# Performance work log

Measured on AMD Instinct MI355X. Metric: run time of the kernel, lower is better.

Reference implementation:

```python
import jax, jax.numpy as jnp
import numpy as np

NUM_HEADS = 16
LN_EPS = 1e-5


def pos_encoding(length, d):
    pos = jnp.arange(length, dtype=jnp.float32)[:, None]
    i = jnp.arange(d, dtype=jnp.float32)[None, :]
    angle = pos / jnp.power(10000.0, (2.0 * jnp.floor(i / 2.0)) / d)
    return jnp.where((jnp.arange(d) % 2) == 0, jnp.sin(angle), jnp.cos(angle))


def rel_shift(x):
    # x: (B, H, l, m) -> TXL shift trick
    b, h, l, m = x.shape
    x = jnp.concatenate([x, jnp.zeros((b, h, l, 1), x.dtype)], axis=-1)
    x = x.reshape(b, h, l * (m + 1))
    return x[:, :, l - 1:-1].reshape(b, h, l, m)


def layer_norm(x, g, b):
    mu = jnp.mean(x, axis=-1, keepdims=True)
    var = jnp.mean(jnp.square(x - mu), axis=-1, keepdims=True)
    return (x - mu) * jax.lax.rsqrt(var + LN_EPS) * g + b


def setup_inputs() -> dict:
    key = jax.random.key(0)
    B, S, M, D, L, V = 2, 1024, 1024, 1024, 4, 32000
    ks = jax.random.split(key, 32)
    s = 0.02
    d = {
        'inputs': jax.random.randint(ks[0], (B, S), 0, V, dtype=jnp.int32),
        'mems': jax.random.normal(ks[1], (L, B, M, D), jnp.float32),
        'emb': jax.random.normal(ks[2], (V, D), jnp.float32) * s,
        'Wq': jax.random.normal(ks[3], (L, D, D), jnp.float32) * s,
        'bq': jnp.zeros((L, D), jnp.float32),
        'Wke': jax.random.normal(ks[4], (L, D, D), jnp.float32) * s,
        'bke': jnp.zeros((L, D), jnp.float32),
        'Wkr': jax.random.normal(ks[5], (L, D, D), jnp.float32) * s,
        'bkr': jnp.zeros((L, D), jnp.float32),
        'Wv': jax.random.normal(ks[6], (L, D, D), jnp.float32) * s,
        'bv': jnp.zeros((L, D), jnp.float32),
        'Wo': jax.random.normal(ks[7], (L, D, D), jnp.float32) * s,
        'bo': jnp.zeros((L, D), jnp.float32),
        'ln1_g': jnp.ones((L, D), jnp.float32),
        'ln1_b': jnp.zeros((L, D), jnp.float32),
        'W1': jax.random.normal(ks[8], (L, D, D), jnp.float32) * s,
        'b1': jnp.zeros((L, D), jnp.float32),
        'W2': jax.random.normal(ks[9], (L, D, D), jnp.float32) * s,
        'b2': jnp.zeros((L, D), jnp.float32),
        'ln2_g': jnp.ones((L, D), jnp.float32),
        'ln2_b': jnp.zeros((L, D), jnp.float32),
        'Wh': jax.random.normal(ks[10], (D, D), jnp.float32) * s,
        'bh': jnp.zeros((D,), jnp.float32),
        'Wf': jax.random.normal(ks[11], (D, V), jnp.float32) * s,
        'bf': jnp.zeros((V,), jnp.float32),
        'next_mem_len': 1024,
    }
    return d


def reference(inputs, mems, emb, Wq, bq, Wke, bke, Wkr, bkr, Wv, bv, Wo, bo,
              ln1_g, ln1_b, W1, b1, W2, b2, ln2_g, ln2_b, Wh, bh, Wf, bf,
              next_mem_len):
    B, S = inputs.shape
    L, _, M, D = mems.shape
    T = M + S
    H = NUM_HEADS
    dh = D // H
    sqrt_dk = jnp.sqrt(jnp.float32(dh))

    rel_enc = pos_encoding(T, D)[::-1]  # (T, D), reversed
    # look-ahead mask: query i may attend key j iff j <= i + M
    mask = (jnp.arange(T)[None, :] > (jnp.arange(S)[:, None] + M)).astype(jnp.float32)
    mask = mask[None, None] * -1e9  # (1,1,S,T)

    x = emb[inputs] * jnp.sqrt(jnp.float32(D))  # (B,S,D)

    for l in range(L):
        x_tilde = jnp.concatenate([mems[l], x], axis=1)  # (B,T,D)
        q = (x @ Wq[l] + bq[l]).reshape(B, S, H, dh).transpose(0, 2, 1, 3)
        k = (x_tilde @ Wke[l] + bke[l]).reshape(B, T, H, dh).transpose(0, 2, 1, 3)
        v = (x_tilde @ Wv[l] + bv[l]).reshape(B, T, H, dh).transpose(0, 2, 1, 3)
        A = jnp.einsum('bhsd,bhtd->bhst', q, k)
        Qr = (rel_enc @ Wkr[l] + bkr[l]).reshape(T, H, dh).transpose(1, 0, 2)  # (H,T,dh)
        B_hat = jnp.einsum('bhsd,htd->bhst', q, Qr)
        score = (A + rel_shift(B_hat)) / sqrt_dk + mask
        attn = jax.nn.softmax(score, axis=-1)
        ctx = jnp.einsum('bhst,bhtd->bhsd', attn, v)
        ctx = ctx.transpose(0, 2, 1, 3).reshape(B, S, D)
        attn_out = ctx @ Wo[l] + bo[l]
        h1 = layer_norm(x + attn_out, ln1_g[l], ln1_b[l])
        ff = jax.nn.gelu(h1 @ W1[l] + b1[l], approximate=False) @ W2[l] + b2[l]
        x = layer_norm(h1 + ff, ln2_g[l], ln2_b[l])

    x = jax.nn.gelu(x @ Wh + bh, approximate=False)
    logits = x @ Wf + bf
    return logits
```

## Files before the change

### kernel.cpp

```cpp
#include <hip/hip_runtime.h>
#include <hip/hip_bf16.h>
#include <math.h>

typedef __attribute__((ext_vector_type(4))) float f32x4;
typedef __attribute__((ext_vector_type(8))) short s16x8;
typedef __attribute__((ext_vector_type(4))) short s16x4;

#define BB 2
#define SS 1024
#define MEM 1024
#define DD 1024
#define LL 4
#define VV 32000
#define TT 2048
#define NH 16
#define DH 64

__device__ __forceinline__ short f2bf(float f) {
    unsigned u = __float_as_uint(f);
    u += 0x7fffu + ((u >> 16) & 1u);
    return (short)(u >> 16);
}

__device__ __forceinline__ float gelu_f(float x) {
    return 0.5f * x * (1.0f + erff(x * 0.70710678118654752f));
}

__device__ __forceinline__ void gll16(const short* g, short* l) {
    __builtin_amdgcn_global_load_lds(
        (__attribute__((address_space(1))) void*)(short*)g,
        (__attribute__((address_space(3))) void*)l, 16, 0, 0);
}

template<int WM, int WN>
__global__ __launch_bounds__(256) void gemm_bf16(
    const short* __restrict__ A, const short* __restrict__ Bt,
    const float* __restrict__ bias, void* __restrict__ Cv,
    int N, int K, int act, int obf)
{
    constexpr int BM = WM * 32, BN = WN * 32;
    constexpr int NA = BM / 32, NB = BN / 32;
    __shared__ short a_s[BM * 64];
    __shared__ short b_s[BN * 64];
    const int tid  = threadIdx.x;
    const int lane = tid & 63;
    const int wave = tid >> 6;
    const int wr = wave >> 1, wc = wave & 1;
    const int fr = lane & 15, fg = lane >> 4;
    const size_t m0 = (size_t)blockIdx.y * BM;
    const size_t n0 = (size_t)blockIdx.x * BN;

    const short* gA[NA]; short* lA[NA];
    const short* gB[NB]; short* lB[NB];
    #pragma unroll
    for (int i = 0; i < NA; ++i) {
        const int s   = i * 256 + tid;
        const int row = (s >> 7) * 16 + (s & 15);
        const int kof = ((s >> 4) & 7) * 8;
        gA[i] = A + (m0 + row) * (size_t)K + kof;
        lA[i] = &a_s[s * 8];
    }
    #pragma unroll
    for (int i = 0; i < NB; ++i) {
        const int s   = i * 256 + tid;
        const int nn  = (s >> 7) * 16 + (s & 15);
        const int kof = ((s >> 4) & 7) * 8;
        gB[i] = Bt + (n0 + nn) * (size_t)K + kof;
        lB[i] = &b_s[s * 8];
    }

    f32x4 acc[WM][WN] = {};

    #pragma unroll
    for (int i = 0; i < NA; ++i) gll16(gA[i], lA[i]);
    #pragma unroll
    for (int i = 0; i < NB; ++i) gll16(gB[i], lB[i]);

    for (int k0 = 0; k0 < K; k0 += 64) {
        __syncthreads();
        s16x8 af[WM][2], bf[WN][2];
        #pragma unroll
        for (int mi = 0; mi < WM; ++mi)
            #pragma unroll
            for (int h = 0; h < 2; ++h)
                af[mi][h] = *(const s16x8*)&a_s[((wr*WM + mi)*128 + (h*4 + fg)*16 + fr) * 8];
        #pragma unroll
        for (int ni = 0; ni < WN; ++ni)
            #pragma unroll
            for (int h = 0; h < 2; ++h)
                bf[ni][h] = *(const s16x8*)&b_s[((wc*WN + ni)*128 + (h*4 + fg)*16 + fr) * 8];
        if (k0 + 64 < K) {
            __syncthreads();
            #pragma unroll
            for (int i = 0; i < NA; ++i) gll16(gA[i] + k0 + 64, lA[i]);
            #pragma unroll
            for (int i = 0; i < NB; ++i) gll16(gB[i] + k0 + 64, lB[i]);
        }
        #pragma unroll
        for (int mi = 0; mi < WM; ++mi)
            #pragma unroll
            for (int ni = 0; ni < WN; ++ni) {
                acc[mi][ni] = __builtin_amdgcn_mfma_f32_16x16x32_bf16(
                    af[mi][0], bf[ni][0], acc[mi][ni], 0, 0, 0);
                acc[mi][ni] = __builtin_amdgcn_mfma_f32_16x16x32_bf16(
                    af[mi][1], bf[ni][1], acc[mi][ni], 0, 0, 0);
            }
    }

    float* Cf = (float*)Cv;
    short* Cb = (short*)Cv;
    #pragma unroll
    for (int mi = 0; mi < WM; ++mi) {
        #pragma unroll
        for (int ni = 0; ni < WN; ++ni) {
            const size_t r0 = m0 + wr*WM*16 + mi*16 + fg*4;
            const size_t c  = n0 + wc*WN*16 + ni*16 + fr;
            const float bb = bias[c];
            #pragma unroll
            for (int rg = 0; rg < 4; ++rg) {
                float vv = acc[mi][ni][rg] + bb;
                if (act) vv = gelu_f(vv);
                if (obf) Cb[(r0 + rg)*(size_t)N + c] = f2bf(vv);
                else     Cf[(r0 + rg)*(size_t)N + c] = vv;
            }
        }
    }
}

__global__ __launch_bounds__(256) void transpose7_kernel(
    const float* w0, const float* w1, const float* w2, const float* w3,
    const float* w4, const float* w5, const float* w6, short* out)
{
    __shared__ float t[32][33];
    const int z = blockIdx.z;
    const float* W;
    switch (z) {
        case 0: W = w0; break; case 1: W = w1; break; case 2: W = w2; break;
        case 3: W = w3; break; case 4: W = w4; break; case 5: W = w5; break;
        default: W = w6; break;
    }
    short* O = out + (size_t)z * DD * DD;
    const int tid = threadIdx.x;
    const int k0 = blockIdx.y * 32, n0 = blockIdx.x * 32;
    const int r = tid >> 3, c4 = (tid & 7) * 4;
    float4 v = *(const float4*)&W[(size_t)(k0 + r) * DD + n0 + c4];
    t[r][c4+0] = v.x; t[r][c4+1] = v.y; t[r][c4+2] = v.z; t[r][c4+3] = v.w;
    __syncthreads();
    short4 o;
    o.x = f2bf(t[c4+0][r]); o.y = f2bf(t[c4+1][r]);
    o.z = f2bf(t[c4+2][r]); o.w = f2bf(t[c4+3][r]);
    *(short4*)&O[(size_t)(n0 + r) * DD + k0 + c4] = o;
}

__global__ __launch_bounds__(256) void transposeF_kernel(
    const float* __restrict__ W, short* __restrict__ O)
{
    __shared__ float t[32][33];
    const int tid = threadIdx.x;
    const int k0 = blockIdx.y * 32, n0 = blockIdx.x * 32;
    const int r = tid >> 3, c4 = (tid & 7) * 4;
    float4 v = *(const float4*)&W[(size_t)(k0 + r) * VV + n0 + c4];
    t[r][c4+0] = v.x; t[r][c4+1] = v.y; t[r][c4+2] = v.z; t[r][c4+3] = v.w;
    __syncthreads();
    short4 o;
    o.x = f2bf(t[c4+0][r]); o.y = f2bf(t[c4+1][r]);
    o.z = f2bf(t[c4+2][r]); o.w = f2bf(t[c4+3][r]);
    *(short4*)&O[(size_t)(n0 + r) * DD + k0 + c4] = o;
}

__global__ __launch_bounds__(256) void attn_kernel(
    const short* __restrict__ q, const short* __restrict__ k,
    const short* __restrict__ v, const short* __restrict__ Qr,
    short* __restrict__ ctx)
{
    __shared__ short q_s[32][72];
    __shared__ short k_s[32][72];
    __shared__ short qr_s[64][72];
    __shared__ short vT_s[64][40];
    __shared__ float a_t[32][37];
    __shared__ float b_t[32][68];
    __shared__ short p_s[32][40];
    __shared__ float row_m[32], row_l[32], row_sc[32];

    const int tid  = threadIdx.x;
    const int id   = blockIdx.x;
    const int bh   = id & 31;
    const int qi   = ((id >> 5) + bh) & 31;
    const int q0   = qi * 32;
    const int b    = bh >> 4;
    const int h    = bh & 15;
    const int hoff = h * DH;

    const int lane = tid & 63;
    const int wave = tid >> 6;
    const int fr   = lane & 15;
    const int fg   = lane >> 4;
    const int mi   = wave >> 1;
    const int nqk  = wave & 1;
    const int nf0  = (wave & 1) * 2;
    const int tk  = tid >> 3;
    const int ck  = (tid & 7) * 8;
    const int iq  = tid >> 2;
    const int cq4 = (tid & 3) * 16;
    const int sr  = tid >> 3;
    const int sc0 = (tid & 7) * 4;

    {
        const short* qp = q + ((size_t)(b * SS + q0 + tk)) * DD + hoff + ck;
        *(s16x8*)&q_s[tk][ck] = *(const s16x8*)qp;
    }
    if (tid < 32) { row_m[tid] = -INFINITY; row_l[tid] = 0.0f; }

    const int t_end  = q0 + 32 + MEM;
    const int u0base = SS - 1 - (q0 + 31);

    s16x8 kf, vf, rfA, rfB;
    auto loadT = [&](int t0) {
        kf = *(const s16x8*)(k + ((size_t)(b * TT + t0 + tk)) * DD + hoff + ck);
        vf = *(const s16x8*)(v + ((size_t)(b * TT + t0 + tk)) * DD + hoff + ck);
        int u = t0 + u0base + iq;
        u = u < 0 ? 0 : (u > TT - 1 ? TT - 1 : u);
        const short* rp = Qr + (size_t)u * DD + hoff + cq4;
        rfA = *(const s16x8*)rp;
        rfB = *(const s16x8*)(rp + 8);
    };
    loadT(0);

    __syncthreads();
    s16x8 aq0 = *(const s16x8*)&q_s[16 * mi + fr][fg * 8];
    s16x8 aq1 = *(const s16x8*)&q_s[16 * mi + fr][32 + fg * 8];

    f32x4 opv0 = {0,0,0,0}, opv1 = {0,0,0,0};

    for (int t0 = 0; t0 < t_end; t0 += 32) {
        __syncthreads();
        {
            *(s16x8*)&k_s[tk][ck] = kf;
            const int tsw = tk ^ (((ck >> 3) & 3) << 3);
            vT_s[ck + 0][tsw] = vf[0];
            vT_s[ck + 1][tsw] = vf[1];
            vT_s[ck + 2][tsw] = vf[2];
            vT_s[ck + 3][tsw] = vf[3];
            vT_s[ck + 4][tsw] = vf[4];
            vT_s[ck + 5][tsw] = vf[5];
            vT_s[ck + 6][tsw] = vf[6];
            vT_s[ck + 7][tsw] = vf[7];
            *(s16x8*)&qr_s[iq][cq4]     = rfA;
            *(s16x8*)&qr_s[iq][cq4 + 8] = rfB;
        }
        if (t0 + 32 < t_end) loadT(t0 + 32);
        __syncthreads();

        {
            s16x8 b0 = *(const s16x8*)&k_s[16 * nqk + fr][fg * 8];
            s16x8 b1 = *(const s16x8*)&k_s[16 * nqk + fr][32 + fg * 8];
            f32x4 ca = {0,0,0,0};
            ca = __builtin_amdgcn_mfma_f32_16x16x32_bf16(aq0, b0, ca, 0, 0, 0);
            ca = __builtin_amdgcn_mfma_f32_16x16x32_bf16(aq1, b1, ca, 0, 0, 0);
            #pragma unroll
            for (int rg = 0; rg < 4; ++rg)
                a_t[16 * mi + 4 * fg + rg][16 * nqk + fr] = ca[rg];
            #pragma unroll
            for (int i = 0; i < 2; ++i) {
                const int nf = nf0 + i;
                s16x8 c0 = *(const s16x8*)&qr_s[16 * nf + fr][fg * 8];
                s16x8 c1 = *(const s16x8*)&qr_s[16 * nf + fr][32 + fg * 8];
                f32x4 cb = {0,0,0,0};
                cb = __builtin_amdgcn_mfma_f32_16x16x32_bf16(aq0, c0, cb, 0, 0, 0);
                cb = __builtin_amdgcn_mfma_f32_16x16x32_bf16(aq1, c1, cb, 0, 0, 0);
                #pragma unroll
                for (int rg = 0; rg < 4; ++rg)
                    b_t[16 * mi + 4 * fg + rg][16 * nf + fr] = cb[rg];
            }
        }
        __syncthreads();

        {
            const int s_glob = q0 + sr;
            float sv[4];
            #pragma unroll
            for (int j = 0; j < 4; ++j) {
                const int c = sc0 + j;
                float scv = (a_t[sr][c] + b_t[sr][c + 31 - sr]) * 0.125f;
                sv[j] = (t0 + c > s_glob + MEM) ? -1e30f : scv;
            }
            float mx = fmaxf(fmaxf(sv[0], sv[1]), fmaxf(sv[2], sv[3]));
            mx = fmaxf(mx, __shfl_xor(mx, 1, 64));
            mx = fmaxf(mx, __shfl_xor(mx, 2, 64));
            mx = fmaxf(mx, __shfl_xor(mx, 4, 64));
            const float mo = row_m[sr];
            const float mn = fmaxf(mo, mx);
            const float scl = __expf(mo - mn);
            float sum = 0.0f;
            s16x4 pp;
            #pragma unroll
            for (int j = 0; j < 4; ++j) {
                float e = __expf(sv[j] - mn);
                sum += e;
                pp[j] = f2bf(e);
            }
            sum += __shfl_xor(sum, 1, 64);
            sum += __shfl_xor(sum, 2, 64);
            sum += __shfl_xor(sum, 4, 64);
            if ((tid & 7) == 0) {
                row_m[sr]  = mn;
                row_sc[sr] = scl;
                row_l[sr]  = row_l[sr] * scl + sum;
            }
            *(s16x4*)&p_s[sr][sc0] = pp;
        }
        __syncthreads();

        {
            f32x4 scv;
            #pragma unroll
            for (int rg = 0; rg < 4; ++rg) scv[rg] = row_sc[16 * mi + 4 * fg + rg];
            #pragma unroll
            for (int rg = 0; rg < 4; ++rg) { opv0[rg] *= scv[rg]; opv1[rg] *= scv[rg]; }
            s16x8 ap = *(const s16x8*)&p_s[16 * mi + fr][fg * 8];
            const int d0 = 16 * nf0 + fr;
            const int d1 = d0 + 16;
            s16x8 bv0 = *(const s16x8*)&vT_s[d0][(fg ^ ((d0 >> 3) & 3)) * 8];
            s16x8 bv1 = *(const s16x8*)&vT_s[d1][(fg ^ ((d1 >> 3) & 3)) * 8];
            opv0 = __builtin_amdgcn_mfma_f32_16x16x32_bf16(ap, bv0, opv0, 0, 0, 0);
            opv1 = __builtin_amdgcn_mfma_f32_16x16x32_bf16(ap, bv1, opv1, 0, 0, 0);
        }
    }

    __syncthreads();
    {
        #pragma unroll
        for (int rg = 0; rg < 4; ++rg) {
            const int row = 16 * mi + 4 * fg + rg;
            const float inv = 1.0f / row_l[row];
            short* op = ctx + ((size_t)(b * SS + q0 + row)) * DD + hoff;
            op[16 * nf0 + fr]      = f2bf(opv0[rg] * inv);
            op[16 * nf0 + 16 + fr] = f2bf(opv1[rg] * inv);
        }
    }
}

__global__ __launch_bounds__(256) void addln_kernel(
    const float* __restrict__ a, const float* __restrict__ b,
    const float* __restrict__ g, const float* __restrict__ be,
    float* __restrict__ out32, short* __restrict__ outbf)
{
    __shared__ float red[8];
    const int row = blockIdx.x;
    const int tid = threadIdx.x;
    const size_t base = (size_t)row * DD;
    const int c = tid * 4;
    float4 xa = *(const float4*)(a + base + c);
    float4 xb = *(const float4*)(b + base + c);
    float x0 = xa.x + xb.x, x1 = xa.y + xb.y, x2 = xa.z + xb.z, x3 = xa.w + xb.w;
    float s  = x0 + x1 + x2 + x3;
    float sq = x0 * x0 + x1 * x1 + x2 * x2 + x3 * x3;
    #pragma unroll
    for (int o = 32; o > 0; o >>= 1) {
        s  += __shfl_down(s, o, 64);
        sq += __shfl_down(sq, o, 64);
    }
    const int wv = tid >> 6;
    if ((tid & 63) == 0) { red[wv * 2] = s; red[wv * 2 + 1] = sq; }
    __syncthreads();
    float ts = red[0] + red[2] + red[4] + red[6];
    float tq = red[1] + red[3] + red[5] + red[7];
    float mu  = ts * (1.0f / DD);
    float var = tq * (1.0f / DD) - mu * mu;
    float rs  = rsqrtf(var + 1e-5f);
    float4 gv = *(const float4*)(g + c);
    float4 bv = *(const float4*)(be + c);
    float4 o4;
    o4.x = (x0 - mu) * rs * gv.x + bv.x;
    o4.y = (x1 - mu) * rs * gv.y + bv.y;
    o4.z = (x2 - mu) * rs * gv.z + bv.z;
    o4.w = (x3 - mu) * rs * gv.w + bv.w;
    *(float4*)(out32 + base + c) = o4;
    short4 ob;
    ob.x = f2bf(o4.x); ob.y = f2bf(o4.y); ob.z = f2bf(o4.z); ob.w = f2bf(o4.w);
    *(short4*)(outbf + base + c) = ob;
}

__global__ __launch_bounds__(256) void embed_kernel(
    const int* __restrict__ inp, const float* __restrict__ emb,
    float* __restrict__ x32, short* __restrict__ xbf)
{
    const int row = blockIdx.x;
    const int c = threadIdx.x * 4;
    const int idx = inp[row];
    float4 vv = *(const float4*)(emb + (size_t)idx * DD + c);
    vv.x *= 32.0f; vv.y *= 32.0f; vv.z *= 32.0f; vv.w *= 32.0f;
    *(float4*)(x32 + (size_t)row * DD + c) = vv;
    short4 ob;
    ob.x = f2bf(vv.x); ob.y = f2bf(vv.y); ob.z = f2bf(vv.z); ob.w = f2bf(vv.w);
    *(short4*)(xbf + (size_t)row * DD + c) = ob;
}

__global__ __launch_bounds__(256) void concat_kernel(
    const float* __restrict__ mems_l, const short* __restrict__ xbf,
    short* __restrict__ xt)
{
    size_t i = ((size_t)blockIdx.x * 256 + threadIdx.x) * 8;
    size_t bt = i / DD;
    int d = (int)(i - bt * DD);
    int b = (int)(bt / TT);
    int t = (int)(bt - (size_t)b * TT);
    s16x8 o;
    if (t < MEM) {
        const float* mp = mems_l + ((size_t)(b * MEM + t)) * DD + d;
        float4 a0 = *(const float4*)mp;
        float4 a1 = *(const float4*)(mp + 4);
        o[0] = f2bf(a0.x); o[1] = f2bf(a0.y); o[2] = f2bf(a0.z); o[3] = f2bf(a0.w);
        o[4] = f2bf(a1.x); o[5] = f2bf(a1.y); o[6] = f2bf(a1.z); o[7] = f2bf(a1.w);
    } else {
        o = *(const s16x8*)(xbf + ((size_t)(b * SS + (t - MEM))) * DD + d);
    }
    *(s16x8*)(xt + i) = o;
}

__global__ __launch_bounds__(256) void relenc_kernel(short* __restrict__ re)
{
    const int u = blockIdx.x;
    const int p = TT - 1 - u;
    const int i0 = threadIdx.x * 4;
    short4 o;
    #pragma unroll
    for (int j = 0; j < 4; ++j) {
        int i = i0 + j;
        float ex   = (float)(2 * (i >> 1)) * (1.0f / DD);
        float invf = __expf(-ex * 9.210340371976184f);
        float ang  = (float)p * invf;
        float val  = (i & 1) ? cosf(ang) : sinf(ang);
        ((short*)&o)[j] = f2bf(val);
    }
    *(short4*)&re[(size_t)u * DD + i0] = o;
}

extern "C" void kernel_launch(void* const* d_in, const int* in_sizes, int n_in,
                              void* d_out, int out_size, void* d_ws, size_t ws_size,
                              hipStream_t stream)
{
    const int*   inp  = (const int*)d_in[0];
    const float* mems = (const float*)d_in[1];
    const float* emb  = (const float*)d_in[2];
    const float* Wq   = (const float*)d_in[3];
    const float* bq   = (const float*)d_in[4];
    const float* Wke  = (const float*)d_in[5];
    const float* bke  = (const float*)d_in[6];
    const float* Wkr  = (const float*)d_in[7];
    const float* bkr  = (const float*)d_in[8];
    const float* Wv   = (const float*)d_in[9];
    const float* bv   = (const float*)d_in[10];
    const float* Wo   = (const float*)d_in[11];
    const float* bo   = (const float*)d_in[12];
    const float* ln1g = (const float*)d_in[13];
    const float* ln1b = (const float*)d_in[14];
    const float* W1   = (const float*)d_in[15];
    const float* b1   = (const float*)d_in[16];
    const float* W2   = (const float*)d_in[17];
    const float* b2   = (const float*)d_in[18];
    const float* ln2g = (const float*)d_in[19];
    const float* ln2b = (const float*)d_in[20];
    const float* Wh   = (const float*)d_in[21];
    const float* bh   = (const float*)d_in[22];
    const float* Wf   = (const float*)d_in[23];
    const float* bfb  = (const float*)d_in[24];

    char* wsb = (char*)d_ws;
    size_t off = 0;
    auto alloc = [&](size_t bytes) { char* p = wsb + off; off += (bytes + 255) & ~(size_t)255; return p; };
    float* h132  = (float*)alloc((size_t)BB*SS*DD*4);
    float* ao32  = (float*)alloc((size_t)BB*SS*DD*4);
    float* ff232 = (float*)alloc((size_t)BB*SS*DD*4);
    short* xt    = (short*)alloc((size_t)BB*TT*DD*2);
    short* qb    = (short*)alloc((size_t)BB*SS*DD*2);
    short* kb    = (short*)alloc((size_t)BB*TT*DD*2);
    short* vbuf  = (short*)alloc((size_t)BB*TT*DD*2);
    short* qr    = (short*)alloc((size_t)TT*DD*2);
    short* ctxb  = (short*)alloc((size_t)BB*SS*DD*2);
    short* ff1   = (short*)alloc((size_t)BB*SS*DD*2);
    float* x32   = (float*)alloc((size_t)BB*SS*DD*4);
    short* x_bf  = (short*)alloc((size_t)BB*SS*DD*2);
    short* whout = (short*)alloc((size_t)BB*SS*DD*2);
    short* rel   = (short*)alloc((size_t)TT*DD*2);
    short* wt7   = (short*)alloc((size_t)7*DD*DD*2);
    short* wft   = (short*)h132;

    relenc_kernel<<<TT, 256, 0, stream>>>(rel);
    embed_kernel<<<BB * SS, 256, 0, stream>>>(inp, emb, x32, x_bf);

    const dim3 gS(DD / 64, (BB * SS) / 64);
    const dim3 gTt(DD / 64, (BB * TT) / 64);
    const dim3 gR(DD / 64, TT / 64);
    const size_t WOFF = (size_t)DD * DD;

    for (int l = 0; l < LL; ++l) {
        const size_t wo  = (size_t)l * DD * DD;
        const size_t bo_ = (size_t)l * DD;
        transpose7_kernel<<<dim3(32, 32, 7), 256, 0, stream>>>(
            Wq + wo, Wke + wo, Wkr + wo, Wv + wo, Wo + wo, W1 + wo, W2 + wo, wt7);
        concat_kernel<<<(BB * TT * DD / 8) / 256, 256, 0, stream>>>(
            mems + (size_t)l * BB * MEM * DD, x_bf, xt);
        gemm_bf16<2,2><<<gS,  256, 0, stream>>>(x_bf, wt7 + 0*WOFF, bq  + bo_, qb,   DD, DD, 0, 1);
        gemm_bf16<2,2><<<gTt, 256, 0, stream>>>(xt,   wt7 + 1*WOFF, bke + bo_, kb,   DD, DD, 0, 1);
        gemm_bf16<2,2><<<gTt, 256, 0, stream>>>(xt,   wt7 + 3*WOFF, bv  + bo_, vbuf, DD, DD, 0, 1);
        gemm_bf16<2,2><<<gR,  256, 0, stream>>>(rel,  wt7 + 2*WOFF, bkr + bo_, qr,   DD, DD, 0, 1);
        attn_kernel<<<dim3((SS / 32) * BB * NH), 256, 0, stream>>>(qb, kb, vbuf, qr, ctxb);
        gemm_bf16<2,2><<<gS, 256, 0, stream>>>(ctxb, wt7 + 4*WOFF, bo + bo_, ao32, DD, DD, 0, 0);
        addln_kernel<<<BB * SS, 256, 0, stream>>>(x32, ao32, ln1g + bo_, ln1b + bo_, h132, (short*)x_bf);
        gemm_bf16<2,2><<<gS, 256, 0, stream>>>(x_bf, wt7 + 5*WOFF, b1 + bo_, ff1,   DD, DD, 1, 1);
        gemm_bf16<2,2><<<gS, 256, 0, stream>>>(ff1,  wt7 + 6*WOFF, b2 + bo_, ff232, DD, DD, 0, 0);
        addln_kernel<<<BB * SS, 256, 0, stream>>>(h132, ff232, ln2g + bo_, ln2b + bo_, x32, x_bf);
    }

    transpose7_kernel<<<dim3(32, 32, 1), 256, 0, stream>>>(
        Wh, Wh, Wh, Wh, Wh, Wh, Wh, wt7);
    transposeF_kernel<<<dim3(VV / 32, DD / 32), 256, 0, stream>>>(Wf, wft);
    gemm_bf16<2,2><<<gS, 256, 0, stream>>>(x_bf, wt7, bh, whout, DD, DD, 1, 1);
    gemm_bf16<4,4><<<dim3(VV / 128, (BB * SS) / 128), 256, 0, stream>>>(
        whout, wft, bfb, (float*)d_out, VV, DD, 0, 0);
}
```

Baseline: 1.549 ms.

## Double-buffer GEMM LDS, enlarge tiles, swizzle grid, fuse K/V projections

The bf16 GEMM now keeps two LDS stages, so the next K-slice prefetch is issued before the current one is read and one barrier per iteration goes away. Most projection GEMMs move from 64x64 to 128x64 tiles, and the two T-length GEMMs use 128x128. Blocks are launched on a 1D grid with a grouped swizzle meant to improve L2 reuse. The K and V projections are fused into one N=2048 GEMM with a split bias, and attention reads them through a strided layout. In exchange, LDS use doubles and grids get smaller, which may lower occupancy.

```diff
diff --git a/kernel.cpp b/kernel.cpp
--- a/kernel.cpp
+++ b/kernel.cpp
@@ -35,20 +35,25 @@
 template<int WM, int WN>
 __global__ __launch_bounds__(256) void gemm_bf16(
     const short* __restrict__ A, const short* __restrict__ Bt,
-    const float* __restrict__ bias, void* __restrict__ Cv,
-    int N, int K, int act, int obf)
+    const float* __restrict__ bias, const float* __restrict__ bias2,
+    int nsplit, void* __restrict__ Cv, int N, int K, int nby, int act, int obf)
 {
     constexpr int BM = WM * 32, BN = WN * 32;
     constexpr int NA = BM / 32, NB = BN / 32;
-    __shared__ short a_s[BM * 64];
-    __shared__ short b_s[BN * 64];
+    constexpr int ASZ = BM * 64, BSZ = BN * 64;
+    __shared__ short a_s[2 * ASZ];
+    __shared__ short b_s[2 * BSZ];
     const int tid  = threadIdx.x;
     const int lane = tid & 63;
     const int wave = tid >> 6;
     const int wr = wave >> 1, wc = wave & 1;
     const int fr = lane & 15, fg = lane >> 4;
-    const size_t m0 = (size_t)blockIdx.y * BM;
-    const size_t n0 = (size_t)blockIdx.x * BN;
+
+    const int nwg = gridDim.x;
+    const int bid = blockIdx.x;
+    const int swz = ((nwg & 7) == 0) ? ((bid & 7) * (nwg >> 3) + (bid >> 3)) : bid;
+    const size_t m0 = (size_t)(swz % nby) * BM;
+    const size_t n0 = (size_t)(swz / nby) * BN;
 
     const short* gA[NA]; short* lA[NA];
     const short* gB[NB]; short* lB[NB];
@@ -76,26 +81,30 @@
     #pragma unroll
     for (int i = 0; i < NB; ++i) gll16(gB[i], lB[i]);
 
-    for (int k0 = 0; k0 < K; k0 += 64) {
+    const int nt = K >> 6;
+    for (int t = 0; t < nt; ++t) {
+        const int cur = t & 1;
         __syncthreads();
+        if (t + 1 < nt) {
+            const int koff = (t + 1) << 6;
+            #pragma unroll
+            for (int i = 0; i < NA; ++i) gll16(gA[i] + koff, lA[i] + (cur ^ 1) * ASZ);
+            #pragma unroll
+            for (int i = 0; i < NB; ++i) gll16(gB[i] + koff, lB[i] + (cur ^ 1) * BSZ);
+        }
+        const short* ab = &a_s[cur * ASZ];
+        const short* bb = &b_s[cur * BSZ];
         s16x8 af[WM][2], bf[WN][2];
         #pragma unroll
         for (int mi = 0; mi < WM; ++mi)
             #pragma unroll
             for (int h = 0; h < 2; ++h)
-                af[mi][h] = *(const s16x8*)&a_s[((wr*WM + mi)*128 + (h*4 + fg)*16 + fr) * 8];
+                af[mi][h] = *(const s16x8*)&ab[((wr*WM + mi)*128 + (h*4 + fg)*16 + fr) * 8];
         #pragma unroll
         for (int ni = 0; ni < WN; ++ni)
             #pragma unroll
             for (int h = 0; h < 2; ++h)
-                bf[ni][h] = *(const s16x8*)&b_s[((wc*WN + ni)*128 + (h*4 + fg)*16 + fr) * 8];
-        if (k0 + 64 < K) {
-            __syncthreads();
-            #pragma unroll
-            for (int i = 0; i < NA; ++i) gll16(gA[i] + k0 + 64, lA[i]);
-            #pragma unroll
-            for (int i = 0; i < NB; ++i) gll16(gB[i] + k0 + 64, lB[i]);
-        }
+                bf[ni][h] = *(const s16x8*)&bb[((wc*WN + ni)*128 + (h*4 + fg)*16 + fr) * 8];
         #pragma unroll
         for (int mi = 0; mi < WM; ++mi)
             #pragma unroll
@@ -115,7 +124,7 @@
         for (int ni = 0; ni < WN; ++ni) {
             const size_t r0 = m0 + wr*WM*16 + mi*16 + fg*4;
             const size_t c  = n0 + wc*WN*16 + ni*16 + fr;
-            const float bb = bias[c];
+            const float bb = (c < (size_t)nsplit) ? bias[c] : bias2[c - nsplit];
             #pragma unroll
             for (int rg = 0; rg < 4; ++rg) {
                 float vv = acc[mi][ni][rg] + bb;
@@ -171,7 +180,7 @@
 __global__ __launch_bounds__(256) void attn_kernel(
     const short* __restrict__ q, const short* __restrict__ k,
     const short* __restrict__ v, const short* __restrict__ Qr,
-    short* __restrict__ ctx)
+    short* __restrict__ ctx, int kstr)
 {
     __shared__ short q_s[32][72];
     __shared__ short k_s[32][72];
@@ -216,8 +225,8 @@
 
     s16x8 kf, vf, rfA, rfB;
     auto loadT = [&](int t0) {
-        kf = *(const s16x8*)(k + ((size_t)(b * TT + t0 + tk)) * DD + hoff + ck);
-        vf = *(const s16x8*)(v + ((size_t)(b * TT + t0 + tk)) * DD + hoff + ck);
+        kf = *(const s16x8*)(k + ((size_t)(b * TT + t0 + tk)) * kstr + hoff + ck);
+        vf = *(const s16x8*)(v + ((size_t)(b * TT + t0 + tk)) * kstr + hoff + ck);
         int u = t0 + u0base + iq;
         u = u < 0 ? 0 : (u > TT - 1 ? TT - 1 : u);
         const short* rp = Qr + (size_t)u * DD + hoff + cq4;
@@ -474,8 +483,7 @@
     float* ff232 = (float*)alloc((size_t)BB*SS*DD*4);
     short* xt    = (short*)alloc((size_t)BB*TT*DD*2);
     short* qb    = (short*)alloc((size_t)BB*SS*DD*2);
-    short* kb    = (short*)alloc((size_t)BB*TT*DD*2);
-    short* vbuf  = (short*)alloc((size_t)BB*TT*DD*2);
+    short* kvb   = (short*)alloc((size_t)BB*TT*DD*2*2);
     short* qr    = (short*)alloc((size_t)TT*DD*2);
     short* ctxb  = (short*)alloc((size_t)BB*SS*DD*2);
     short* ff1   = (short*)alloc((size_t)BB*SS*DD*2);
@@ -489,34 +497,35 @@
     relenc_kernel<<<TT, 256, 0, stream>>>(rel);
     embed_kernel<<<BB * SS, 256, 0, stream>>>(inp, emb, x32, x_bf);
 
-    const dim3 gS(DD / 64, (BB * SS) / 64);
-    const dim3 gTt(DD / 64, (BB * TT) / 64);
-    const dim3 gR(DD / 64, TT / 64);
     const size_t WOFF = (size_t)DD * DD;
+    const int gS   = (DD / 64) * ((BB * SS) / 128);
+    const int gKV  = ((2 * DD) / 128) * ((BB * TT) / 128);
+    const int nbyS = (BB * SS) / 128;
+    const int nbyKV= (BB * TT) / 128;
 
     for (int l = 0; l < LL; ++l) {
         const size_t wo  = (size_t)l * DD * DD;
         const size_t bo_ = (size_t)l * DD;
         transpose7_kernel<<<dim3(32, 32, 7), 256, 0, stream>>>(
-            Wq + wo, Wke + wo, Wkr + wo, Wv + wo, Wo + wo, W1 + wo, W2 + wo, wt7);
+            Wq + wo, Wke + wo, Wv + wo, Wkr + wo, Wo + wo, W1 + wo, W2 + wo, wt7);
         concat_kernel<<<(BB * TT * DD / 8) / 256, 256, 0, stream>>>(
             mems + (size_t)l * BB * MEM * DD, x_bf, xt);
-        gemm_bf16<2,2><<<gS,  256, 0, stream>>>(x_bf, wt7 + 0*WOFF, bq  + bo_, qb,   DD, DD, 0, 1);
-        gemm_bf16<2,2><<<gTt, 256, 0, stream>>>(xt,   wt7 + 1*WOFF, bke + bo_, kb,   DD, DD, 0, 1);
-        gemm_bf16<2,2><<<gTt, 256, 0, stream>>>(xt,   wt7 + 3*WOFF, bv  + bo_, vbuf, DD, DD, 0, 1);
-        gemm_bf16<2,2><<<gR,  256, 0, stream>>>(rel,  wt7 + 2*WOFF, bkr + bo_, qr,   DD, DD, 0, 1);
-        attn_kernel<<<dim3((SS / 32) * BB * NH), 256, 0, stream>>>(qb, kb, vbuf, qr, ctxb);
-        gemm_bf16<2,2><<<gS, 256, 0, stream>>>(ctxb, wt7 + 4*WOFF, bo + bo_, ao32, DD, DD, 0, 0);
+        gemm_bf16<4,2><<<gS,  256, 0, stream>>>(x_bf, wt7 + 0*WOFF, bq + bo_, bq + bo_, DD, qb, DD, DD, nbyS, 0, 1);
+        gemm_bf16<4,4><<<gKV, 256, 0, stream>>>(xt,   wt7 + 1*WOFF, bke + bo_, bv + bo_, DD, kvb, 2*DD, DD, nbyKV, 0, 1);
+        gemm_bf16<4,2><<<gS,  256, 0, stream>>>(rel,  wt7 + 3*WOFF, bkr + bo_, bkr + bo_, DD, qr, DD, DD, nbyS, 0, 1);
+        attn_kernel<<<dim3((SS / 32) * BB * NH), 256, 0, stream>>>(
+            qb, kvb, kvb + DD, qr, ctxb, 2 * DD);
+        gemm_bf16<4,2><<<gS, 256, 0, stream>>>(ctxb, wt7 + 4*WOFF, bo + bo_, bo + bo_, DD, ao32, DD, DD, nbyS, 0, 0);
         addln_kernel<<<BB * SS, 256, 0, stream>>>(x32, ao32, ln1g + bo_, ln1b + bo_, h132, (short*)x_bf);
-        gemm_bf16<2,2><<<gS, 256, 0, stream>>>(x_bf, wt7 + 5*WOFF, b1 + bo_, ff1,   DD, DD, 1, 1);
-        gemm_bf16<2,2><<<gS, 256, 0, stream>>>(ff1,  wt7 + 6*WOFF, b2 + bo_, ff232, DD, DD, 0, 0);
+        gemm_bf16<4,2><<<gS, 256, 0, stream>>>(x_bf, wt7 + 5*WOFF, b1 + bo_, b1 + bo_, DD, ff1,   DD, DD, nbyS, 1, 1);
+        gemm_bf16<4,2><<<gS, 256, 0, stream>>>(ff1,  wt7 + 6*WOFF, b2 + bo_, b2 + bo_, DD, ff232, DD, DD, nbyS, 0, 0);
         addln_kernel<<<BB * SS, 256, 0, stream>>>(h132, ff232, ln2g + bo_, ln2b + bo_, x32, x_bf);
     }
 
     transpose7_kernel<<<dim3(32, 32, 1), 256, 0, stream>>>(
         Wh, Wh, Wh, Wh, Wh, Wh, Wh, wt7);
     transposeF_kernel<<<dim3(VV / 32, DD / 32), 256, 0, stream>>>(Wf, wft);
-    gemm_bf16<2,2><<<gS, 256, 0, stream>>>(x_bf, wt7, bh, whout, DD, DD, 1, 1);
-    gemm_bf16<4,4><<<dim3(VV / 128, (BB * SS) / 128), 256, 0, stream>>>(
-        whout, wft, bfb, (float*)d_out, VV, DD, 0, 0);
-}
+    gemm_bf16<4,2><<<gS, 256, 0, stream>>>(x_bf, wt7, bh, bh, DD, whout, DD, DD, nbyS, 1, 1);
+    gemm_bf16<4,4><<<dim3((VV / 128) * ((BB * SS) / 128)), 256, 0, stream>>>(
+        whout, wft, bfb, bfb, VV, (float*)d_out, VV, DD, (BB * SS) / 128, 0, 0);
+}
```

Measured after the change: 1.596 ms. 3.0% more time.
